# Kernel optimization log

Measured on AMD Instinct MI355X. Metric: run time of the kernel, lower is better.

## Reference

```python
import jax, jax.numpy as jnp
import numpy as np

BS, S, DIM, H = 4, 2048, 768, 12
DH = DIM // H  # 64


def setup_inputs() -> dict:
    key = jax.random.key(0)
    ks = jax.random.split(key, 12)
    std = 0.02
    inp = {
        "query": jax.random.normal(ks[0], (BS, S, DIM), jnp.float32),
        "key_t": jax.random.normal(ks[1], (BS, S, DIM), jnp.float32),
        "value": jax.random.normal(ks[2], (BS, S, DIM), jnp.float32),
        "mask": jnp.ones((BS, S), jnp.int32),
        "q_w": jax.random.normal(ks[3], (DIM, DIM), jnp.float32) * std,
        "q_b": jnp.zeros((DIM,), jnp.float32),
        "k_w": jax.random.normal(ks[4], (DIM, DIM), jnp.float32) * std,
        "k_b": jnp.zeros((DIM,), jnp.float32),
        "v_w": jax.random.normal(ks[5], (DIM, DIM), jnp.float32) * std,
        "v_b": jnp.zeros((DIM,), jnp.float32),
        "o_w": jax.random.normal(ks[6], (DIM, DIM), jnp.float32) * std,
        "o_b": jnp.zeros((DIM,), jnp.float32),
    }
    return inp


def _shape(x, bs):
    # (bs, L, dim) -> (bs, H, L, DH)
    return x.reshape(bs, -1, H, DH).transpose(0, 2, 1, 3)


def reference(query, key_t, value, mask, q_w, q_b, k_w, k_b, v_w, v_b, o_w, o_b):
    bs, q_len, _ = query.shape
    k_len = key_t.shape[1]
    q = _shape(query @ q_w.T + q_b, bs)   # (bs,H,Sq,DH)
    k = _shape(key_t @ k_w.T + k_b, bs)   # (bs,H,Sk,DH)
    v = _shape(value @ v_w.T + v_b, bs)
    q = q * (1.0 / jnp.sqrt(jnp.asarray(DH, q.dtype)))
    scores = jnp.einsum("bhqd,bhkd->bhqk", q, k)  # (bs,H,Sq,Sk)
    pad = (mask == 0)[:, None, None, :]           # (bs,1,1,Sk)
    neg = jnp.finfo(scores.dtype).min
    scores = jnp.where(pad, neg, scores)
    weights = jax.nn.softmax(scores, axis=-1)
    context = jnp.einsum("bhqk,bhkd->bhqd", weights, v)
    context = context.transpose(0, 2, 1, 3).reshape(bs, q_len, H * DH)
    out = context @ o_w.T + o_b
    return out
```

## Files before the change

kernel.cpp:

```cpp
#include <hip/hip_runtime.h>


#define BSZ 4
#define SEQ 2048
#define DIMD 768
#define NHD 12
#define MTOT (BSZ*SEQ)
#define WELEM (DIMD*DIMD)

typedef __bf16 bf16;
typedef __attribute__((ext_vector_type(8))) __bf16 bf16x8;
typedef __attribute__((ext_vector_type(4))) __bf16 bf16x4;
typedef __attribute__((ext_vector_type(4))) float f32x4;

__device__ __forceinline__ f32x4 mfma_bf16(bf16x8 a, bf16x8 b, f32x4 c) {
    return __builtin_amdgcn_mfma_f32_16x16x32_bf16(a, b, c, 0, 0, 0);
}

__device__ __forceinline__ void async16(const bf16* g, bf16* l) {
    __builtin_amdgcn_global_load_lds(
        (const __attribute__((address_space(1))) unsigned int*)g,
        (__attribute__((address_space(3))) unsigned int*)l, 16, 0, 0);
}

__global__ __launch_bounds__(256) void convert_all_kernel(
    const float* __restrict__ w0, const float* __restrict__ w1,
    const float* __restrict__ w2, const float* __restrict__ w3,
    const float* __restrict__ x0, const float* __restrict__ x1,
    const float* __restrict__ x2,
    bf16* __restrict__ W, bf16* __restrict__ d0, bf16* __restrict__ d1,
    bf16* __restrict__ d2) {
    int id = blockIdx.x;
    const float* src;
    bf16* dst;
    int base;
    if (id < 2304) {
        const int z = id / 576, r = id - z * 576;
        src = (z == 0) ? w0 : (z == 1) ? w1 : (z == 2) ? w2 : w3;
        dst = W + (size_t)z * WELEM;
        base = r * 1024;
    } else {
        id -= 2304;
        const int z = id / 6144, r = id - z * 6144;
        src = (z == 0) ? x0 : (z == 1) ? x1 : x2;
        dst = (z == 0) ? d0 : (z == 1) ? d1 : d2;
        base = r * 1024;
    }
    const int i = base + threadIdx.x * 4;
    float4 v = *(const float4*)(src + i);
    bf16x4 o;
    o[0] = (bf16)v.x; o[1] = (bf16)v.y; o[2] = (bf16)v.z; o[3] = (bf16)v.w;
    *(bf16x4*)(dst + i) = o;
}

__device__ __forceinline__ void gemm_core_768(
    const bf16* __restrict__ Ag, const bf16* __restrict__ Bg,
    int m0, int n0, bf16* As, bf16* Bs, f32x4 (&acc)[4][4]) {
    const int tid = threadIdx.x;
    const int lane = tid & 63, wv = tid >> 6;
    const int quad = lane >> 4, l16 = lane & 15;
    const int wr = wv >> 1, wc = wv & 1;
    const int rr = lane >> 3, cbl = lane & 7;
    const int swz = l16 & 7;
    for (int kt = 0; kt < 12; ++kt) {
        if (kt) __syncthreads();
        for (int c = 0; c < 4; ++c) {
            const int row = c * 32 + wv * 8 + rr;
            const int cb = cbl ^ (row & 7);
            const size_t gcol = (size_t)kt * 64 + cb * 8;
            async16(Ag + (size_t)(m0 + row) * 768 + gcol, As + row * 64 + cbl * 8);
            async16(Bg + (size_t)(n0 + row) * 768 + gcol, Bs + row * 64 + cbl * 8);
        }
        __syncthreads();
        for (int ks = 0; ks < 2; ++ks) {
            bf16x8 af[4], bfr[4];
            for (int t = 0; t < 4; ++t)
                af[t] = *(const bf16x8*)(As + (wr * 64 + t * 16 + l16) * 64 +
                                         (((ks * 4 + quad) ^ swz) * 8));
            for (int t = 0; t < 4; ++t)
                bfr[t] = *(const bf16x8*)(Bs + (wc * 64 + t * 16 + l16) * 64 +
                                          (((ks * 4 + quad) ^ swz) * 8));
            __builtin_amdgcn_s_setprio(1);
            for (int ti = 0; ti < 4; ++ti)
                for (int tj = 0; tj < 4; ++tj)
                    acc[ti][tj] = mfma_bf16(af[ti], bfr[tj], acc[ti][tj]);
            __builtin_amdgcn_s_setprio(0);
        }
    }
}

#define OTS 136

__global__ __launch_bounds__(256, 2) void proj_kernel(
    const bf16* __restrict__ Xq, const bf16* __restrict__ Xk, const bf16* __restrict__ Xv,
    const bf16* __restrict__ W,
    const float* __restrict__ bq, const float* __restrict__ bk, const float* __restrict__ bv,
    bf16* __restrict__ Qo, bf16* __restrict__ Ko, bf16* __restrict__ Vo) {
    __shared__ __align__(16) bf16 smem[128 * OTS];
    bf16* As = smem;
    bf16* Bs = smem + 128 * 64;
    const int lin = blockIdx.x;
    const int swzb = (lin & 7) * 144 + (lin >> 3);
    const int z = swzb / 384;
    const int rem = swzb - z * 384;
    const int rt = rem / 6;
    const int xt = rem - rt * 6;
    const bf16* X = (z == 0) ? Xq : (z == 1) ? Xk : Xv;
    const bf16* Wz = W + (size_t)z * WELEM;
    const float* bias = (z == 0) ? bq : (z == 1) ? bk : bv;
    bf16* Out = (z == 0) ? Qo : (z == 1) ? Ko : Vo;

    const int tid = threadIdx.x;
    const int lane = tid & 63, wv = tid >> 6;
    const int quad = lane >> 4, l16 = lane & 15;
    const int wr = wv >> 1, wc = wv & 1;
    f32x4 acc[4][4] = {};
    int m0, n0;
    const bf16 *Ag, *Bg;
    if (z < 2) { m0 = xt * 128; n0 = rt * 128; Ag = Wz; Bg = X; }
    else       { m0 = rt * 128; n0 = xt * 128; Ag = X;  Bg = Wz; }
    gemm_core_768(Ag, Bg, m0, n0, As, Bs, acc);
    __syncthreads();
    bf16* Ot = smem;
    if (z < 2) {
        const float scale = (z == 0) ? 0.18033688011112042f : 1.0f;
        for (int ti = 0; ti < 4; ++ti) {
            const int featl = wr * 64 + ti * 16 + quad * 4;
            const float4 b4 = *(const float4*)(bias + m0 + featl);
            for (int tj = 0; tj < 4; ++tj) {
                const int sl = wc * 64 + tj * 16 + l16;
                bf16x4 pk;
                pk[0] = (bf16)((acc[ti][tj][0] + b4.x) * scale);
                pk[1] = (bf16)((acc[ti][tj][1] + b4.y) * scale);
                pk[2] = (bf16)((acc[ti][tj][2] + b4.z) * scale);
                pk[3] = (bf16)((acc[ti][tj][3] + b4.w) * scale);
                *(bf16x4*)&Ot[sl * OTS + featl] = pk;
            }
        }
        __syncthreads();
        for (int it = 0; it < 8; ++it) {
            const int unit = it * 256 + tid;
            const int s = unit >> 4, u = unit & 15;
            const int feat = m0 + u * 8;
            const int hh = feat >> 6, dh = feat & 63;
            const int srow = n0 + s;
            const int bb = srow >> 11, s2 = srow & 2047;
            *(bf16x8*)&Out[((size_t)(bb * NHD + hh) * SEQ + s2) * 64 + dh] =
                *(const bf16x8*)&Ot[s * OTS + u * 8];
        }
    } else {
        for (int ti = 0; ti < 4; ++ti) {
            const int sl = wr * 64 + ti * 16 + quad * 4;
            for (int tj = 0; tj < 4; ++tj) {
                const int featl = wc * 64 + tj * 16 + l16;
                const float bv = bias[n0 + featl];
                bf16x4 pk;
                pk[0] = (bf16)(acc[ti][tj][0] + bv);
                pk[1] = (bf16)(acc[ti][tj][1] + bv);
                pk[2] = (bf16)(acc[ti][tj][2] + bv);
                pk[3] = (bf16)(acc[ti][tj][3] + bv);
                *(bf16x4*)&Ot[featl * OTS + sl] = pk;
            }
        }
        __syncthreads();
        const int bb = m0 >> 11, sbase = m0 & 2047;
        for (int it = 0; it < 8; ++it) {
            const int unit = it * 256 + tid;
            const int fl = unit >> 4, u = unit & 15;
            const int feat = n0 + fl;
            const int hh = feat >> 6, dh = feat & 63;
            *(bf16x8*)&Out[((size_t)(bb * NHD + hh) * 64 + dh) * SEQ + sbase + u * 8] =
                *(const bf16x8*)&Ot[fl * OTS + u * 8];
        }
    }
}

__global__ __launch_bounds__(256, 2) void attn_kernel(
    const bf16* __restrict__ Qb, const bf16* __restrict__ Kb, const bf16* __restrict__ Vb,
    const int* __restrict__ mask, bf16* __restrict__ CTX) {
    __shared__ __align__(16) bf16 Ks[2][64][64];
    __shared__ __align__(16) bf16 Vs[2][64][64];
    __shared__ __align__(16) bf16 Ps[4][32][64];
    __shared__ int anyz_s;
    const int tid = threadIdx.x;
    const int lane = tid & 63, wv = tid >> 6, quad = lane >> 4, l16 = lane & 15;
    const int swz = l16 & 7;
    const int lin = blockIdx.x;
    const int nb = (lin & 7) * 96 + (lin >> 3);
    const int qt = nb & 15;
    const int bh = nb >> 4;
    const int b = bh / NHD, h = bh - b * NHD;
    if (tid == 0) anyz_s = 0;
    __syncthreads();
    {
        int4 m0v = *(const int4*)(mask + b * SEQ + tid * 8);
        int4 m1v = *(const int4*)(mask + b * SEQ + tid * 8 + 4);
        if (!(m0v.x && m0v.y && m0v.z && m0v.w && m1v.x && m1v.y && m1v.z && m1v.w))
            anyz_s = 1;
    }
    bf16x8 qf0[2], qf1[2];
    for (int st = 0; st < 2; ++st) {
        const bf16* qp = Qb + ((size_t)bh * SEQ + qt * 128 + wv * 32 + st * 16 + l16) * 64;
        qf0[st] = *(const bf16x8*)(qp + quad * 8);
        qf1[st] = *(const bf16x8*)(qp + 32 + quad * 8);
    }
    const bf16* Kg = Kb + (size_t)bh * SEQ * 64;
    const bf16* Vg = Vb + (size_t)bh * 64 * SEQ;
    const int* Mp = mask + b * SEQ;
    bf16* Pw = &Ps[wv][0][0];
    f32x4 acc[2][4] = {};
    float rm[2] = {-1e30f, -1e30f}, rs[2] = {0.f, 0.f};

    const int s_sub = lane >> 3;
    const int s_row = wv * 8 + s_sub;
    const int s_dst = (lane & 7) * 8;
    const int s_src = ((lane & 7) ^ s_sub) * 8;
#define STAGE_KV(BUF, K0) do {                                                 \
        async16(Kg + (size_t)((K0) + s_row) * 64 + s_src,                      \
                &Ks[BUF][s_row][s_dst]);                                       \
        async16(Kg + (size_t)((K0) + 32 + s_row) * 64 + s_src,                 \
                &Ks[BUF][32 + s_row][s_dst]);                                  \
        async16(Vg + (size_t)s_row * SEQ + (K0) + s_src,                       \
                &Vs[BUF][s_row][s_dst]);                                       \
        async16(Vg + (size_t)(32 + s_row) * SEQ + (K0) + s_src,                \
                &Vs[BUF][32 + s_row][s_dst]);                                  \
    } while (0)

    STAGE_KV(0, 0);
    __syncthreads();
    const int az = anyz_s;

    for (int kt = 0; kt < SEQ / 64; ++kt) {
        const int cur = kt & 1, k0 = kt * 64;
        const int kn = (kt < SEQ / 64 - 1) ? k0 + 64 : k0;
        STAGE_KV(cur ^ 1, kn);
        bf16x8 kf0[4], kf1[4];
        #pragma unroll
        for (int jj = 0; jj < 4; ++jj) {
            const bf16* kr = &Ks[cur][jj * 16 + l16][0];
            kf0[jj] = *(const bf16x8*)(kr + ((quad ^ swz) * 8));
            kf1[jj] = *(const bf16x8*)(kr + (((4 + quad) ^ swz) * 8));
        }
        #pragma unroll
        for (int st = 0; st < 2; ++st) {
            f32x4 sc[4];
            __builtin_amdgcn_s_setprio(1);
            #pragma unroll
            for (int jj = 0; jj < 4; ++jj) {
                f32x4 zf = {};
                zf = mfma_bf16(kf0[jj], qf0[st], zf);
                sc[jj] = mfma_bf16(kf1[jj], qf1[st], zf);
            }
            __builtin_amdgcn_s_setprio(0);
            if (az) {
                #pragma unroll
                for (int jj = 0; jj < 4; ++jj) {
                    const int4 mm = *(const int4*)(Mp + k0 + jj * 16 + quad * 4);
                    sc[jj][0] += mm.x ? 0.f : -1e30f;
                    sc[jj][1] += mm.y ? 0.f : -1e30f;
                    sc[jj][2] += mm.z ? 0.f : -1e30f;
                    sc[jj][3] += mm.w ? 0.f : -1e30f;
                }
            }
            float t01 = fmaxf(fmaxf(sc[0][0], sc[0][1]), fmaxf(sc[0][2], sc[0][3]));
            float t23 = fmaxf(fmaxf(sc[1][0], sc[1][1]), fmaxf(sc[1][2], sc[1][3]));
            float t45 = fmaxf(fmaxf(sc[2][0], sc[2][1]), fmaxf(sc[2][2], sc[2][3]));
            float t67 = fmaxf(fmaxf(sc[3][0], sc[3][1]), fmaxf(sc[3][2], sc[3][3]));
            const float tmax = fmaxf(fmaxf(t01, t23), fmaxf(t45, t67));
            if (__any(tmax > rm[st] + 8.0f)) {
                float fm = fmaxf(tmax, __shfl_xor(tmax, 16));
                fm = fmaxf(fm, __shfl_xor(fm, 32));
                const float nmax = fmaxf(rm[st], fm);
                const float alpha = exp2f(rm[st] - nmax);
                rm[st] = nmax;
                rs[st] *= alpha;
                #pragma unroll
                for (int d = 0; d < 4; ++d) {
                    acc[st][d][0] *= alpha; acc[st][d][1] *= alpha;
                    acc[st][d][2] *= alpha; acc[st][d][3] *= alpha;
                }
            }
            float tsum = 0.f;
            const float m = rm[st];
            #pragma unroll
            for (int jj = 0; jj < 4; ++jj) {
                bf16x4 pk;
                #pragma unroll
                for (int r = 0; r < 4; ++r) {
                    const float p = exp2f(sc[jj][r] - m);
                    tsum += p;
                    pk[r] = (bf16)p;
                }
                *(bf16x4*)&Pw[(st * 16 + l16) * 64 + ((jj * 16 + quad * 4) ^ (swz * 8))] = pk;
            }
            rs[st] += tsum;
        }
        bf16x8 vf[4][2];
        #pragma unroll
        for (int d = 0; d < 4; ++d) {
            const bf16* vr = &Vs[cur][d * 16 + l16][0];
            #pragma unroll
            for (int kb = 0; kb < 2; ++kb)
                vf[d][kb] = *(const bf16x8*)(vr + (((kb * 4 + quad) ^ swz) * 8));
        }
        bf16x8 pf[2][2];
        #pragma unroll
        for (int st = 0; st < 2; ++st)
            #pragma unroll
            for (int kb = 0; kb < 2; ++kb)
                pf[st][kb] = *(const bf16x8*)&Pw[(st * 16 + l16) * 64 +
                                                (((kb * 4 + quad) ^ swz) * 8)];
        __builtin_amdgcn_s_setprio(1);
        #pragma unroll
        for (int st = 0; st < 2; ++st)
            #pragma unroll
            for (int kb = 0; kb < 2; ++kb)
                #pragma unroll
                for (int d = 0; d < 4; ++d)
                    acc[st][d] = mfma_bf16(vf[d][kb], pf[st][kb], acc[st][d]);
        __builtin_amdgcn_s_setprio(0);
        __syncthreads();
    }
#undef STAGE_KV

    #pragma unroll
    for (int st = 0; st < 2; ++st) {
        float r = rs[st];
        r += __shfl_xor(r, 16);
        r += __shfl_xor(r, 32);
        const float inv = 1.0f / r;
        const int s = qt * 128 + wv * 32 + st * 16 + l16;
        #pragma unroll
        for (int d = 0; d < 4; ++d) {
            bf16x4 pk;
            #pragma unroll
            for (int rr2 = 0; rr2 < 4; ++rr2) pk[rr2] = (bf16)(acc[st][d][rr2] * inv);
            *(bf16x4*)&CTX[(size_t)(b * SEQ + s) * DIMD + h * 64 + d * 16 + quad * 4] = pk;
        }
    }
}

__global__ __launch_bounds__(256, 2) void oproj_kernel(
    const bf16* __restrict__ ctx, const bf16* __restrict__ wo,
    const float* __restrict__ bo, float* __restrict__ out) {
    __shared__ __align__(16) bf16 smem[2 * 128 * 64];
    const int lin = blockIdx.x;
    const int swzb = (lin & 7) * 48 + (lin >> 3);
    const int rt = swzb / 6;
    const int xt = swzb - rt * 6;
    const int tid = threadIdx.x;
    const int lane = tid & 63, wv = tid >> 6;
    const int quad = lane >> 4, l16 = lane & 15;
    const int wr = wv >> 1, wc = wv & 1;
    const int m0 = rt * 128, n0 = xt * 128;
    f32x4 acc[4][4] = {};
    gemm_core_768(ctx, wo, m0, n0, smem, smem + 128 * 64, acc);
    for (int ti = 0; ti < 4; ++ti) {
        const int rowb = m0 + wr * 64 + ti * 16 + quad * 4;
        for (int tj = 0; tj < 4; ++tj) {
            const int feat = n0 + wc * 64 + tj * 16 + l16;
            const float bv = bo[feat];
            for (int r = 0; r < 4; ++r)
                out[(size_t)(rowb + r) * DIMD + feat] = acc[ti][tj][r] + bv;
        }
    }
}

extern "C" void kernel_launch(void* const* d_in, const int* in_sizes, int n_in,
                              void* d_out, int out_size, void* d_ws, size_t ws_size,
                              hipStream_t stream) {
    const float* query = (const float*)d_in[0];
    const float* key_t = (const float*)d_in[1];
    const float* value = (const float*)d_in[2];
    const int*   mask  = (const int*)d_in[3];
    const float* q_w = (const float*)d_in[4];
    const float* q_b = (const float*)d_in[5];
    const float* k_w = (const float*)d_in[6];
    const float* k_b = (const float*)d_in[7];
    const float* v_w = (const float*)d_in[8];
    const float* v_b = (const float*)d_in[9];
    const float* o_w = (const float*)d_in[10];
    const float* o_b = (const float*)d_in[11];
    float* out = (float*)d_out;

    bf16* ws  = (bf16*)d_ws;
    bf16* W   = ws;
    bf16* XBq = ws + (size_t)4 * WELEM;
    bf16* XBk = XBq + (size_t)MTOT * DIMD;
    bf16* XBv = XBk + (size_t)MTOT * DIMD;
    bf16* Qb  = XBv + (size_t)MTOT * DIMD;
    bf16* Kb  = Qb + (size_t)MTOT * DIMD;
    bf16* Vb  = Kb + (size_t)MTOT * DIMD;
    bf16* CTX = XBq;

    convert_all_kernel<<<2304 + 3 * 6144, 256, 0, stream>>>(
        q_w, k_w, v_w, o_w, query, key_t, value, W, XBq, XBk, XBv);

    proj_kernel<<<1152, 256, 0, stream>>>(XBq, XBk, XBv, W, q_b, k_b, v_b, Qb, Kb, Vb);

    attn_kernel<<<768, 256, 0, stream>>>(Qb, Kb, Vb, mask, CTX);
    oproj_kernel<<<384, 256, 0, stream>>>(CTX, W + (size_t)3 * WELEM, o_b, out);
}
```

Measured before the change: 289.2 us.

## Double-buffer GEMM K-loop with async LDS prefetch and 32-wide K tiles

The shared GEMM core used by the QKV and output projections now uses two LDS buffers with a K step of 32 instead of a single buffer with a K step of 64. The next tile's async global-to-LDS loads are issued before computing on the current tile, with explicit vmcnt waits and raw barriers, so memory latency overlaps with MFMA work. A new XOR swizzle suits the 32-column rows. In exchange there are twice as many loop iterations and barriers, and the final iteration issues a redundant reload of the last tile.

Result: slower. 306.1 us (+5.8%).

```diff
diff --git a/kernel.cpp b/kernel.cpp
--- a/kernel.cpp
+++ b/kernel.cpp
@@ -55,38 +55,55 @@
 
 __device__ __forceinline__ void gemm_core_768(
     const bf16* __restrict__ Ag, const bf16* __restrict__ Bg,
-    int m0, int n0, bf16* As, bf16* Bs, f32x4 (&acc)[4][4]) {
+    int m0, int n0, bf16* smem, f32x4 (&acc)[4][4]) {
     const int tid = threadIdx.x;
     const int lane = tid & 63, wv = tid >> 6;
     const int quad = lane >> 4, l16 = lane & 15;
     const int wr = wv >> 1, wc = wv & 1;
-    const int rr = lane >> 3, cbl = lane & 7;
-    const int swz = l16 & 7;
-    for (int kt = 0; kt < 12; ++kt) {
-        if (kt) __syncthreads();
-        for (int c = 0; c < 4; ++c) {
-            const int row = c * 32 + wv * 8 + rr;
-            const int cb = cbl ^ (row & 7);
-            const size_t gcol = (size_t)kt * 64 + cb * 8;
-            async16(Ag + (size_t)(m0 + row) * 768 + gcol, As + row * 64 + cbl * 8);
-            async16(Bg + (size_t)(n0 + row) * 768 + gcol, Bs + row * 64 + cbl * 8);
-        }
-        __syncthreads();
-        for (int ks = 0; ks < 2; ++ks) {
-            bf16x8 af[4], bfr[4];
-            for (int t = 0; t < 4; ++t)
-                af[t] = *(const bf16x8*)(As + (wr * 64 + t * 16 + l16) * 64 +
-                                         (((ks * 4 + quad) ^ swz) * 8));
-            for (int t = 0; t < 4; ++t)
-                bfr[t] = *(const bf16x8*)(Bs + (wc * 64 + t * 16 + l16) * 64 +
-                                          (((ks * 4 + quad) ^ swz) * 8));
-            __builtin_amdgcn_s_setprio(1);
-            for (int ti = 0; ti < 4; ++ti)
-                for (int tj = 0; tj < 4; ++tj)
-                    acc[ti][tj] = mfma_bf16(af[ti], bfr[tj], acc[ti][tj]);
-            __builtin_amdgcn_s_setprio(0);
-        }
-    }
+    const int r4 = lane >> 2;
+    const int u  = lane & 3;
+    const int row0 = wv * 32 + r4;
+    const int row1 = wv * 32 + 16 + r4;
+    const int src0 = (u ^ (row0 & 3) ^ ((row0 >> 2) & 3)) * 8;
+    const int src1 = (u ^ (row1 & 3) ^ ((row1 >> 2) & 3)) * 8;
+    const int dst0 = row0 * 32 + u * 8;
+    const int dst1 = row1 * 32 + u * 8;
+    const int rsw = (l16 & 3) ^ ((l16 >> 2) & 3);
+    bf16* As[2] = {smem, smem + 4096};
+    bf16* Bs[2] = {smem + 8192, smem + 12288};
+#define G_STAGE(BUF, KC) do {                                                  \
+        async16(Ag + (size_t)(m0 + row0) * 768 + (KC) + src0, As[BUF] + dst0); \
+        async16(Ag + (size_t)(m0 + row1) * 768 + (KC) + src1, As[BUF] + dst1); \
+        async16(Bg + (size_t)(n0 + row0) * 768 + (KC) + src0, Bs[BUF] + dst0); \
+        async16(Bg + (size_t)(n0 + row1) * 768 + (KC) + src1, Bs[BUF] + dst1); \
+    } while (0)
+    G_STAGE(0, 0);
+    for (int kt = 0; kt < 24; ++kt) {
+        const int cur = kt & 1, nxt = cur ^ 1;
+        const int kn = (kt < 23) ? (kt + 1) * 32 : kt * 32;
+        G_STAGE(nxt, kn);
+        asm volatile("s_waitcnt vmcnt(4)" ::: "memory");
+        __builtin_amdgcn_s_barrier();
+        __builtin_amdgcn_sched_barrier(0);
+        bf16x8 af[4], bfr[4];
+        #pragma unroll
+        for (int t = 0; t < 4; ++t)
+            af[t] = *(const bf16x8*)(As[cur] + (wr * 64 + t * 16 + l16) * 32 +
+                                     ((quad ^ rsw) * 8));
+        #pragma unroll
+        for (int t = 0; t < 4; ++t)
+            bfr[t] = *(const bf16x8*)(Bs[cur] + (wc * 64 + t * 16 + l16) * 32 +
+                                      ((quad ^ rsw) * 8));
+        __builtin_amdgcn_s_setprio(1);
+        #pragma unroll
+        for (int ti = 0; ti < 4; ++ti)
+            #pragma unroll
+            for (int tj = 0; tj < 4; ++tj)
+                acc[ti][tj] = mfma_bf16(af[ti], bfr[tj], acc[ti][tj]);
+        __builtin_amdgcn_s_setprio(0);
+        __builtin_amdgcn_s_barrier();
+    }
+#undef G_STAGE
 }
 
 #define OTS 136
@@ -97,8 +114,6 @@
     const float* __restrict__ bq, const float* __restrict__ bk, const float* __restrict__ bv,
     bf16* __restrict__ Qo, bf16* __restrict__ Ko, bf16* __restrict__ Vo) {
     __shared__ __align__(16) bf16 smem[128 * OTS];
-    bf16* As = smem;
-    bf16* Bs = smem + 128 * 64;
     const int lin = blockIdx.x;
     const int swzb = (lin & 7) * 144 + (lin >> 3);
     const int z = swzb / 384;
@@ -119,7 +134,7 @@
     const bf16 *Ag, *Bg;
     if (z < 2) { m0 = xt * 128; n0 = rt * 128; Ag = Wz; Bg = X; }
     else       { m0 = rt * 128; n0 = xt * 128; Ag = X;  Bg = Wz; }
-    gemm_core_768(Ag, Bg, m0, n0, As, Bs, acc);
+    gemm_core_768(Ag, Bg, m0, n0, smem, acc);
     __syncthreads();
     bf16* Ot = smem;
     if (z < 2) {
@@ -343,7 +358,7 @@
 __global__ __launch_bounds__(256, 2) void oproj_kernel(
     const bf16* __restrict__ ctx, const bf16* __restrict__ wo,
     const float* __restrict__ bo, float* __restrict__ out) {
-    __shared__ __align__(16) bf16 smem[2 * 128 * 64];
+    __shared__ __align__(16) bf16 smem[4 * 4096];
     const int lin = blockIdx.x;
     const int swzb = (lin & 7) * 48 + (lin >> 3);
     const int rt = swzb / 6;
@@ -354,7 +369,7 @@
     const int wr = wv >> 1, wc = wv & 1;
     const int m0 = rt * 128, n0 = xt * 128;
     f32x4 acc[4][4] = {};
-    gemm_core_768(ctx, wo, m0, n0, smem, smem + 128 * 64, acc);
+    gemm_core_768(ctx, wo, m0, n0, smem, acc);
     for (int ti = 0; ti < 4; ++ti) {
         const int rowb = m0 + wr * 64 + ti * 16 + quad * 4;
         for (int tj = 0; tj < 4; ++tj) {
```
